# Kernel tuning notes

Measured on AMD Instinct MI355X. Metric: run time of the kernel, lower is better.

## Reference

```python
import jax, jax.numpy as jnp
import numpy as np

HIDDEN = 1024
NUM_HEADS = 4
HEAD_DIM = HIDDEN // NUM_HEADS
SCALE = HEAD_DIM ** -0.5
EPS = 1e-5


def setup_inputs() -> dict:
    key = jax.random.key(0)
    ks = jax.random.split(key, 8)
    B, S, D = 4, 2048, HIDDEN
    x = jax.random.normal(ks[0], (B, S, D), dtype=jnp.float32)
    attention_mask = jnp.ones((B, S), dtype=jnp.int32)
    init = 1.0 / np.sqrt(D)
    Wq = jax.random.uniform(ks[1], (D, D), jnp.float32, -init, init)
    Wk = jax.random.uniform(ks[2], (D, D), jnp.float32, -init, init)
    Wv = jax.random.uniform(ks[3], (D, D), jnp.float32, -init, init)
    Wo = jax.random.uniform(ks[4], (D, D), jnp.float32, -init, init)
    bo = jax.random.uniform(ks[5], (D,), jnp.float32, -init, init)
    gamma = jnp.ones((D,), dtype=jnp.float32)
    beta = jnp.zeros((D,), dtype=jnp.float32)
    return {"x": x, "attention_mask": attention_mask, "Wq": Wq, "Wk": Wk,
            "Wv": Wv, "Wo": Wo, "bo": bo, "gamma": gamma, "beta": beta}


def reference(x, attention_mask, Wq, Wk, Wv, Wo, bo, gamma, beta):
    # Linear layers: y = x @ W^T (torch nn.Linear convention), no bias for q/k/v
    q = jnp.einsum('bsd,ed->bse', x, Wq)
    k = jnp.einsum('bsd,ed->bse', x, Wk)
    v = jnp.einsum('bsd,ed->bse', x, Wv)
    # Full-width attention (module never splits heads), scale = head_dim^-0.5
    scores = jnp.einsum('bqd,bkd->bqk', q, k) * SCALE  # [B,S,S]
    mask = attention_mask[:, None, :]  # [B,1,S]
    scores = jnp.where(mask == 0, jnp.float32(-1e9), scores)
    attn = jax.nn.softmax(scores, axis=-1)
    ctx = jnp.einsum('bqk,bkd->bqd', attn, v)
    out = jnp.einsum('bsd,ed->bse', ctx, Wo) + bo
    # residual + LayerNorm
    h = out + x
    mu = jnp.mean(h, axis=-1, keepdims=True)
    var = jnp.mean(jnp.square(h - mu), axis=-1, keepdims=True)
    return (h - mu) * jax.lax.rsqrt(var + EPS) * gamma + beta
```

## Files before the change

### kernel.cpp

```cpp
#include <hip/hip_runtime.h>

typedef __bf16 bf16;
typedef __bf16 bf16x8 __attribute__((ext_vector_type(8)));
typedef __bf16 bf16x4 __attribute__((ext_vector_type(4)));
typedef float floatx4 __attribute__((ext_vector_type(4)));

#define HIDDEN 1024
#define SEQ 2048
#define BATCH 4
#define ATT_SCALE 0.0625f
#define LN_EPS 1e-5f

__device__ __forceinline__ void gload_lds16(const void* g, void* l) {
    __builtin_amdgcn_global_load_lds(
        (const __attribute__((address_space(1))) unsigned int*)g,
        (__attribute__((address_space(3))) unsigned int*)l, 16, 0, 0);
}

#define GBAR() asm volatile("s_barrier" ::: "memory")
#define MFMA(a, b, c) __builtin_amdgcn_mfma_f32_16x16x32_bf16(a, b, c, 0, 0, 0)

__global__ void cvt_f32_bf16(const float* __restrict__ in, bf16* __restrict__ out, int n4) {
    int i = blockIdx.x * blockDim.x + threadIdx.x;
    if (i >= n4) return;
    float4 v = ((const float4*)in)[i];
    bf16x4 o;
    o[0] = (bf16)v.x; o[1] = (bf16)v.y; o[2] = (bf16)v.z; o[3] = (bf16)v.w;
    ((bf16x4*)out)[i] = o;
}

__global__ void transpose_w3(const float* __restrict__ s0, const float* __restrict__ s1,
                             const float* __restrict__ s2,
                             bf16* __restrict__ d0p, bf16* __restrict__ d1p, bf16* __restrict__ d2p) {
    const float* in = (blockIdx.z == 0) ? s0 : (blockIdx.z == 1) ? s1 : s2;
    bf16* out = (blockIdx.z == 0) ? d0p : (blockIdx.z == 1) ? d1p : d2p;
    __shared__ __attribute__((aligned(16))) bf16 tile[64][72];
    const int d0 = blockIdx.x * 64;
    const int f0 = blockIdx.y * 64;
    const int t = threadIdx.x;
    const int r = t >> 4;
    const int c = (t & 15) * 4;
#pragma unroll
    for (int i = 0; i < 4; ++i) {
        float4 v = *(const float4*)&in[(long)(f0 + r + i * 16) * HIDDEN + d0 + c];
        bf16x4 b;
        b[0] = (bf16)v.x; b[1] = (bf16)v.y; b[2] = (bf16)v.z; b[3] = (bf16)v.w;
        *(bf16x4*)&tile[r + i * 16][c] = b;
    }
    __syncthreads();
#pragma unroll
    for (int i = 0; i < 4; ++i) {
        const int dr = r + i * 16;
        bf16x4 o;
#pragma unroll
        for (int j = 0; j < 4; ++j) o[j] = tile[c + j][dr];
        *(bf16x4*)&out[(long)(d0 + dr) * HIDDEN + f0 + c] = o;
    }
}

template <int BNv, int MODE>
__global__ __launch_bounds__(512, 2)
void gemm256(const bf16* A, const bf16* Bw, void* __restrict__ Cout,
             const float* __restrict__ bias, const float* __restrict__ resid,
             int lda, int ldb, int ldc, int K, float scale,
             long sA, long sB, long sC) {
    constexpr int ABY = 256 * 128;
    constexpr int BBY = BNv * 128;
    constexpr int SLOT = ABY + BBY;
    constexpr int AU = ABY / 8192;
    constexpr int BU = BBY / 8192;
    constexpr int WNc = (BNv == 256) ? 4 : 2;
    constexpr int MR = (BNv == 256) ? 8 : 4;
    constexpr int MH = MR / 2;

    __shared__ __attribute__((aligned(16))) char lds[2 * SLOT];

    const int gx = gridDim.x;
    const int nblk = gx * gridDim.y;
    const int bid = blockIdx.y * gx + blockIdx.x;
    const int cpx = nblk >> 3;
    const int sbid = (nblk & 7) ? bid : (bid & 7) * cpx + (bid >> 3);
    const int bx = sbid % gx, by = sbid / gx;

    const int z = blockIdx.z;
    const char* Ab = (const char*)(A + (long)z * sA);
    const char* Bb = (const char*)(Bw + (long)z * sB);
    const long lda2 = lda * 2L, ldb2 = ldb * 2L;

    const int t = threadIdx.x;
    const int lane = t & 63;
    const int w = t >> 6;
    const int wm = w / WNc, wn = w % WNc;
    const int l15 = lane & 15;
    const int l4 = lane >> 4;

    const int row0 = by * 256;
    const int col0 = bx * BNv;

    const int srow = t >> 3;
    const int soff = (((t & 7) - (srow & 7)) & 7) * 16;
    const char* aP = Ab + (long)(row0 + srow) * lda2 + soff;
    const char* bP = Bb + (long)(col0 + srow) * ldb2 + soff;
    const int ld16 = t * 16;

    auto STAGE = [&](int slot, long koff) {
        char* base = &lds[slot * SLOT];
#pragma unroll
        for (int u = 0; u < AU; ++u)
            gload_lds16(aP + u * 64 * lda2 + koff, base + u * 8192 + ld16);
#pragma unroll
        for (int u = 0; u < BU; ++u)
            gload_lds16(bP + u * 64 * ldb2 + koff, base + ABY + u * 8192 + ld16);
    };

    floatx4 acc[MR][4] = {};
    const int nk = K / 64;

    STAGE(0, 0);
    asm volatile("s_waitcnt vmcnt(0)" ::: "memory");
    GBAR();

    for (int tt = 0; tt < nk; ++tt) {
        const char* sb = &lds[(tt & 1) * SLOT];

        auto RDA = [&](int m, int kkh) {
            int lr = wm * (MR * 16) + m * 16 + l15;
            return *(const bf16x8*)(sb + lr * 128 + (((kkh * 4 + l4 + lr) & 7) << 4));
        };
        auto RDB = [&](int n, int kkh) {
            int lr = wn * 64 + n * 16 + l15;
            return *(const bf16x8*)(sb + ABY + lr * 128 + (((kkh * 4 + l4 + lr) & 7) << 4));
        };

        bf16x8 alo[MH][2], ahi[MH][2], b0[2][2], b1[2][2];
#pragma unroll
        for (int m = 0; m < MH; ++m) { alo[m][0] = RDA(m, 0); alo[m][1] = RDA(m, 1); }
#pragma unroll
        for (int n = 0; n < 2; ++n) {
            b0[n][0] = RDB(n, 0); b0[n][1] = RDB(n, 1);
            b1[n][0] = RDB(2 + n, 0); b1[n][1] = RDB(2 + n, 1);
        }

        if (tt + 1 < nk) STAGE((tt + 1) & 1, (long)(tt + 1) * 128);

        __builtin_amdgcn_s_setprio(1);
#pragma unroll
        for (int m = 0; m < MH; ++m)
#pragma unroll
            for (int n = 0; n < 2; ++n) {
                acc[m][n] = MFMA(alo[m][0], b0[n][0], acc[m][n]);
                acc[m][n] = MFMA(alo[m][1], b0[n][1], acc[m][n]);
            }
        __builtin_amdgcn_s_setprio(0);

#pragma unroll
        for (int m = 0; m < MH; ++m) { ahi[m][0] = RDA(MH + m, 0); ahi[m][1] = RDA(MH + m, 1); }

        __builtin_amdgcn_s_setprio(1);
#pragma unroll
        for (int m = 0; m < MH; ++m)
#pragma unroll
            for (int n = 0; n < 2; ++n) {
                acc[m][2 + n] = MFMA(alo[m][0], b1[n][0], acc[m][2 + n]);
                acc[m][2 + n] = MFMA(alo[m][1], b1[n][1], acc[m][2 + n]);
            }
#pragma unroll
        for (int m = 0; m < MH; ++m)
#pragma unroll
            for (int n = 0; n < 2; ++n) {
                acc[MH + m][n] = MFMA(ahi[m][0], b0[n][0], acc[MH + m][n]);
                acc[MH + m][n] = MFMA(ahi[m][1], b0[n][1], acc[MH + m][n]);
            }
#pragma unroll
        for (int m = 0; m < MH; ++m)
#pragma unroll
            for (int n = 0; n < 2; ++n) {
                acc[MH + m][2 + n] = MFMA(ahi[m][0], b1[n][0], acc[MH + m][2 + n]);
                acc[MH + m][2 + n] = MFMA(ahi[m][1], b1[n][1], acc[MH + m][2 + n]);
            }
        __builtin_amdgcn_s_setprio(0);

        asm volatile("s_waitcnt vmcnt(0)" ::: "memory");
        GBAR();
    }

    const int rq = l4 * 4;
    if constexpr (MODE == 0) {
        bf16* C = ((bf16*)Cout) + (long)z * sC;
#pragma unroll
        for (int m = 0; m < MR; ++m)
#pragma unroll
            for (int i = 0; i < 4; ++i) {
                long gr = row0 + wm * (MR * 16) + m * 16 + rq + i;
#pragma unroll
                for (int n = 0; n < 4; ++n) {
                    int gc = col0 + wn * 64 + n * 16 + l15;
                    C[gr * ldc + gc] = (bf16)(acc[m][n][i] * scale);
                }
            }
    } else {
        float* C = (float*)Cout + (long)z * sC;
        const float* R = resid + (long)z * sC;
#pragma unroll
        for (int m = 0; m < MR; ++m)
#pragma unroll
            for (int i = 0; i < 4; ++i) {
                long gr = row0 + wm * (MR * 16) + m * 16 + rq + i;
#pragma unroll
                for (int n = 0; n < 4; ++n) {
                    int gc = col0 + wn * 64 + n * 16 + l15;
                    C[gr * ldc + gc] = acc[m][n][i] + bias[gc] + R[gr * ldc + gc];
                }
            }
    }
}

__global__ void transpose_v(const bf16* __restrict__ yv, bf16* __restrict__ out) {
    __shared__ __attribute__((aligned(16))) bf16 tile[64][72];
    const int z = blockIdx.z;
    const bf16* ib = yv + (long)z * SEQ * 2048 + 1024;
    bf16* ob = out + (long)z * SEQ * HIDDEN;
    const int d0 = blockIdx.x * 64;
    const int s0 = blockIdx.y * 64;
    const int t = threadIdx.x;
    const int r = t >> 4;
    const int c = (t & 15) * 4;
#pragma unroll
    for (int i = 0; i < 4; ++i) {
        bf16x4 v = *(const bf16x4*)&ib[(long)(s0 + r + i * 16) * 2048 + d0 + c];
        *(bf16x4*)&tile[r + i * 16][c] = v;
    }
    __syncthreads();
#pragma unroll
    for (int i = 0; i < 4; ++i) {
        const int dr = r + i * 16;
        bf16x4 o;
#pragma unroll
        for (int j = 0; j < 4; ++j) o[j] = tile[c + j][dr];
        *(bf16x4*)&ob[(long)(d0 + dr) * SEQ + s0 + c] = o;
    }
}

__global__ void softmax_rows(bf16* __restrict__ S, const int* __restrict__ mask) {
    const int b = blockIdx.y;
    const int row = blockIdx.x;
    bf16* srow = S + ((long)b * SEQ + row) * SEQ;
    const int* mrow = mask + b * SEQ;
    const int t = threadIdx.x;

    bf16x8 sv = *(const bf16x8*)&srow[t * 8];
    int4 m0 = ((const int4*)mrow)[t * 2];
    int4 m1 = ((const int4*)mrow)[t * 2 + 1];
    int mk[8] = {m0.x, m0.y, m0.z, m0.w, m1.x, m1.y, m1.z, m1.w};

    float v[8];
    float mx = -1e30f;
#pragma unroll
    for (int j = 0; j < 8; ++j) {
        float s = (float)sv[j];
        if (mk[j] == 0) s = -1e9f;
        v[j] = s;
        mx = fmaxf(mx, s);
    }
    __shared__ float redm[4], reds[4];
#pragma unroll
    for (int off = 32; off > 0; off >>= 1) mx = fmaxf(mx, __shfl_down(mx, off));
    if ((t & 63) == 0) redm[t >> 6] = mx;
    __syncthreads();
    mx = fmaxf(fmaxf(redm[0], redm[1]), fmaxf(redm[2], redm[3]));

    float sum = 0.f;
#pragma unroll
    for (int j = 0; j < 8; ++j) {
        v[j] = __expf(v[j] - mx);
        sum += v[j];
    }
#pragma unroll
    for (int off = 32; off > 0; off >>= 1) sum += __shfl_down(sum, off);
    if ((t & 63) == 0) reds[t >> 6] = sum;
    __syncthreads();
    sum = reds[0] + reds[1] + reds[2] + reds[3];
    float inv = 1.0f / sum;

    bf16x8 o;
#pragma unroll
    for (int j = 0; j < 8; ++j) o[j] = (bf16)(v[j] * inv);
    *(bf16x8*)&srow[t * 8] = o;
}

__global__ void layernorm_out(const float* __restrict__ h, const float* __restrict__ gamma,
                              const float* __restrict__ beta, float* __restrict__ out) {
    const long row = blockIdx.x;
    const float* hr = h + row * HIDDEN;
    const int t = threadIdx.x;
    float4 v = ((const float4*)hr)[t];
    float s = v.x + v.y + v.z + v.w;
    float sq = v.x * v.x + v.y * v.y + v.z * v.z + v.w * v.w;
    __shared__ float rs[4], rq[4];
#pragma unroll
    for (int off = 32; off > 0; off >>= 1) {
        s += __shfl_down(s, off);
        sq += __shfl_down(sq, off);
    }
    if ((t & 63) == 0) { rs[t >> 6] = s; rq[t >> 6] = sq; }
    __syncthreads();
    s = rs[0] + rs[1] + rs[2] + rs[3];
    sq = rq[0] + rq[1] + rq[2] + rq[3];
    float mu = s * (1.0f / HIDDEN);
    float var = sq * (1.0f / HIDDEN) - mu * mu;
    float rinv = rsqrtf(var + LN_EPS);
    float4 g = ((const float4*)gamma)[t];
    float4 bt = ((const float4*)beta)[t];
    float4 o;
    o.x = (v.x - mu) * rinv * g.x + bt.x;
    o.y = (v.y - mu) * rinv * g.y + bt.y;
    o.z = (v.z - mu) * rinv * g.z + bt.z;
    o.w = (v.w - mu) * rinv * g.w + bt.w;
    ((float4*)(out + row * HIDDEN))[t] = o;
}

extern "C" void kernel_launch(void* const* d_in, const int* in_sizes, int n_in,
                              void* d_out, int out_size, void* d_ws, size_t ws_size,
                              hipStream_t stream) {
    const float* x     = (const float*)d_in[0];
    const int*   mask  = (const int*)d_in[1];
    const float* Wq    = (const float*)d_in[2];
    const float* Wk    = (const float*)d_in[3];
    const float* Wv    = (const float*)d_in[4];
    const float* Wo    = (const float*)d_in[5];
    const float* bo    = (const float*)d_in[6];
    const float* gamma = (const float*)d_in[7];
    const float* beta  = (const float*)d_in[8];
    float* out = (float*)d_out;

    char* ws = (char*)d_ws;
    const long MB = 1024L * 1024L;
    bf16* yv   = (bf16*)(ws + 0 * MB);
    float* h   = (float*)(ws + 0 * MB);
    bf16* xb   = (bf16*)(ws + 32 * MB);
    bf16* vt   = (bf16*)(ws + 48 * MB);
    bf16* wgc  = (bf16*)(ws + 64 * MB);
    bf16* wkT  = (bf16*)(ws + 68 * MB);
    bf16* wo   = (bf16*)(ws + 70 * MB);
    bf16* wqT  = (bf16*)(ws + 72 * MB);
    bf16* wvT  = (bf16*)(ws + 74 * MB);
    bf16* S    = (bf16*)(ws + 76 * MB);

    const int BS = BATCH * SEQ;
    const int WW = HIDDEN * HIDDEN;
    dim3 blk256(256), blk512(512);

    cvt_f32_bf16<<<dim3(BS * HIDDEN / 4 / 256), blk256, 0, stream>>>(x, xb, BS * HIDDEN / 4);
    cvt_f32_bf16<<<dim3(WW / 4 / 256), blk256, 0, stream>>>(Wo, wo, WW / 4);
    transpose_w3<<<dim3(16, 16, 3), blk256, 0, stream>>>(Wq, Wk, Wv, wqT, wkT, wvT);

    gemm256<128, 0><<<dim3(HIDDEN / 128, HIDDEN / 256, 2), blk512, 0, stream>>>(
        wkT, wqT, wgc, nullptr, nullptr, HIDDEN, HIDDEN, HIDDEN, HIDDEN, 1.0f,
        (long)WW, (long)WW, (long)WW);

    gemm256<256, 0><<<dim3(2048 / 256, BS / 256, 1), blk512, 0, stream>>>(
        xb, wgc, yv, nullptr, nullptr, HIDDEN, HIDDEN, 2048, HIDDEN, 1.0f, 0, 0, 0);

    transpose_v<<<dim3(HIDDEN / 64, SEQ / 64, BATCH), blk256, 0, stream>>>(yv, vt);

    gemm256<256, 0><<<dim3(SEQ / 256, SEQ / 256, BATCH), blk512, 0, stream>>>(
        yv, xb, S, nullptr, nullptr, 2048, HIDDEN, SEQ, HIDDEN, ATT_SCALE,
        (long)SEQ * 2048, (long)SEQ * HIDDEN, (long)SEQ * SEQ);

    softmax_rows<<<dim3(SEQ, BATCH), blk256, 0, stream>>>(S, mask);

    gemm256<128, 2><<<dim3(HIDDEN / 128, SEQ / 256, BATCH), blk512, 0, stream>>>(
        S, vt, h, bo, x, SEQ, SEQ, HIDDEN, SEQ, 1.0f,
        (long)SEQ * SEQ, (long)HIDDEN * SEQ, (long)SEQ * HIDDEN);

    layernorm_out<<<dim3(BS), blk256, 0, stream>>>(h, gamma, beta, out);
}
```

Before: 181.3 us.

## Split-K the weight-product and PV GEMMs, move bias and residual into LayerNorm

The Wk^T·Wq product GEMM is split four ways along K into fp32 partials, which a new reduce kernel sums into bf16. The attention-times-V GEMM is split in two along K, writing bf16 partials. The bias, residual add and partial summation move into the LayerNorm kernel. The goal is more blocks for under-filled grids on many CUs, at the cost of extra partial-buffer traffic, an extra launch, and bf16 rounding of the partials.

```diff
diff --git a/kernel.cpp b/kernel.cpp
--- a/kernel.cpp
+++ b/kernel.cpp
@@ -10,6 +10,7 @@
 #define BATCH 4
 #define ATT_SCALE 0.0625f
 #define LN_EPS 1e-5f
+#define WW (HIDDEN * HIDDEN)
 
 __device__ __forceinline__ void gload_lds16(const void* g, void* l) {
     __builtin_amdgcn_global_load_lds(
@@ -61,9 +62,8 @@
 template <int BNv, int MODE>
 __global__ __launch_bounds__(512, 2)
 void gemm256(const bf16* A, const bf16* Bw, void* __restrict__ Cout,
-             const float* __restrict__ bias, const float* __restrict__ resid,
              int lda, int ldb, int ldc, int K, float scale,
-             long sA, long sB, long sC) {
+             long sA, long sB, long sC, int zmod) {
     constexpr int ABY = 256 * 128;
     constexpr int BBY = BNv * 128;
     constexpr int SLOT = ABY + BBY;
@@ -83,8 +83,9 @@
     const int bx = sbid % gx, by = sbid / gx;
 
     const int z = blockIdx.z;
-    const char* Ab = (const char*)(A + (long)z * sA);
-    const char* Bb = (const char*)(Bw + (long)z * sB);
+    const int mat = z % zmod, ks = z / zmod;
+    const char* Ab = (const char*)(A + (long)mat * sA + (long)ks * K);
+    const char* Bb = (const char*)(Bw + (long)mat * sB + (long)ks * K);
     const long lda2 = lda * 2L, ldb2 = ldb * 2L;
 
     const int t = threadIdx.x;
@@ -200,7 +201,6 @@
             }
     } else {
         float* C = (float*)Cout + (long)z * sC;
-        const float* R = resid + (long)z * sC;
 #pragma unroll
         for (int m = 0; m < MR; ++m)
 #pragma unroll
@@ -209,10 +209,73 @@
 #pragma unroll
                 for (int n = 0; n < 4; ++n) {
                     int gc = col0 + wn * 64 + n * 16 + l15;
-                    C[gr * ldc + gc] = acc[m][n][i] + bias[gc] + R[gr * ldc + gc];
+                    C[gr * ldc + gc] = acc[m][n][i];
                 }
             }
     }
+}
+
+__global__ void reduce_wgc(const float* __restrict__ p, bf16* __restrict__ out) {
+    int i = blockIdx.x * blockDim.x + threadIdx.x;
+    int e = i * 4;
+    int mat = e >> 20;
+    int local = e & (WW - 1);
+    float4 s = *(const float4*)(p + (long)mat * WW + local);
+#pragma unroll
+    for (int ksp = 1; ksp < 4; ++ksp) {
+        float4 a = *(const float4*)(p + (long)(ksp * 2 + mat) * WW + local);
+        s.x += a.x; s.y += a.y; s.z += a.z; s.w += a.w;
+    }
+    bf16x4 o;
+    o[0] = (bf16)s.x; o[1] = (bf16)s.y; o[2] = (bf16)s.z; o[3] = (bf16)s.w;
+    *(bf16x4*)&out[e] = o;
+}
+
+__global__ void softmax_rows(bf16* __restrict__ S, const int* __restrict__ mask) {
+    const int b = blockIdx.y;
+    const int row = blockIdx.x;
+    bf16* srow = S + ((long)b * SEQ + row) * SEQ;
+    const int* mrow = mask + b * SEQ;
+    const int t = threadIdx.x;
+
+    bf16x8 sv = *(const bf16x8*)&srow[t * 8];
+    int4 m0 = ((const int4*)mrow)[t * 2];
+    int4 m1 = ((const int4*)mrow)[t * 2 + 1];
+    int mk[8] = {m0.x, m0.y, m0.z, m0.w, m1.x, m1.y, m1.z, m1.w};
+
+    float v[8];
+    float mx = -1e30f;
+#pragma unroll
+    for (int j = 0; j < 8; ++j) {
+        float s = (float)sv[j];
+        if (mk[j] == 0) s = -1e9f;
+        v[j] = s;
+        mx = fmaxf(mx, s);
+    }
+    __shared__ float redm[4], reds[4];
+#pragma unroll
+    for (int off = 32; off > 0; off >>= 1) mx = fmaxf(mx, __shfl_down(mx, off));
+    if ((t & 63) == 0) redm[t >> 6] = mx;
+    __syncthreads();
+    mx = fmaxf(fmaxf(redm[0], redm[1]), fmaxf(redm[2], redm[3]));
+
+    float sum = 0.f;
+#pragma unroll
+    for (int j = 0; j < 8; ++j) {
+        v[j] = __expf(v[j] - mx);
+        sum += v[j];
+    }
+#pragma unroll
+    for (int off = 32; off > 0; off >>= 1) sum += __shfl_down(sum, off);
+    if ((t & 63) == 0) reds[t >> 6] = sum;
+    __syncthreads();
+    sum = reds[0] + reds[1] + reds[2] + reds[3];
+    float inv = 1.0f / sum;
+
+    bf16x8 o;
+#pragma unroll
+    for (int j = 0; j < 8; ++j) o[j] = (bf16)(v[j] * inv);
+    *(bf16x8*)&srow[t * 8] = o;
 }
 
 __global__ void transpose_v(const bf16* __restrict__ yv, bf16* __restrict__ out) {
@@ -241,72 +304,39 @@
     }
 }
 
-__global__ void softmax_rows(bf16* __restrict__ S, const int* __restrict__ mask) {
-    const int b = blockIdx.y;
-    const int row = blockIdx.x;
-    bf16* srow = S + ((long)b * SEQ + row) * SEQ;
-    const int* mrow = mask + b * SEQ;
-    const int t = threadIdx.x;
-
-    bf16x8 sv = *(const bf16x8*)&srow[t * 8];
-    int4 m0 = ((const int4*)mrow)[t * 2];
-    int4 m1 = ((const int4*)mrow)[t * 2 + 1];
-    int mk[8] = {m0.x, m0.y, m0.z, m0.w, m1.x, m1.y, m1.z, m1.w};
-
-    float v[8];
-    float mx = -1e30f;
-#pragma unroll
-    for (int j = 0; j < 8; ++j) {
-        float s = (float)sv[j];
-        if (mk[j] == 0) s = -1e9f;
-        v[j] = s;
-        mx = fmaxf(mx, s);
-    }
-    __shared__ float redm[4], reds[4];
-#pragma unroll
-    for (int off = 32; off > 0; off >>= 1) mx = fmaxf(mx, __shfl_down(mx, off));
-    if ((t & 63) == 0) redm[t >> 6] = mx;
-    __syncthreads();
-    mx = fmaxf(fmaxf(redm[0], redm[1]), fmaxf(redm[2], redm[3]));
-
-    float sum = 0.f;
-#pragma unroll
-    for (int j = 0; j < 8; ++j) {
-        v[j] = __expf(v[j] - mx);
-        sum += v[j];
-    }
-#pragma unroll
-    for (int off = 32; off > 0; off >>= 1) sum += __shfl_down(sum, off);
-    if ((t & 63) == 0) reds[t >> 6] = sum;
-    __syncthreads();
-    sum = reds[0] + reds[1] + reds[2] + reds[3];
-    float inv = 1.0f / sum;
-
-    bf16x8 o;
-#pragma unroll
-    for (int j = 0; j < 8; ++j) o[j] = (bf16)(v[j] * inv);
-    *(bf16x8*)&srow[t * 8] = o;
-}
-
-__global__ void layernorm_out(const float* __restrict__ h, const float* __restrict__ gamma,
+__global__ void layernorm_out(const bf16* __restrict__ pp, const float* __restrict__ x,
+                              const float* __restrict__ bo, const float* __restrict__ gamma,
                               const float* __restrict__ beta, float* __restrict__ out) {
     const long row = blockIdx.x;
-    const float* hr = h + row * HIDDEN;
+    const int b = (int)(row >> 11);
+    const int s = (int)(row & 2047);
+    const bf16* r0 = pp + ((long)b * SEQ + s) * HIDDEN;
+    const bf16* r1 = r0 + 4L * SEQ * HIDDEN;
     const int t = threadIdx.x;
-    float4 v = ((const float4*)hr)[t];
-    float s = v.x + v.y + v.z + v.w;
+
+    bf16x4 a0 = ((const bf16x4*)r0)[t];
+    bf16x4 a1 = ((const bf16x4*)r1)[t];
+    float4 xv = ((const float4*)(x + row * HIDDEN))[t];
+    float4 bv = ((const float4*)bo)[t];
+    float4 v;
+    v.x = (float)a0[0] + (float)a1[0] + bv.x + xv.x;
+    v.y = (float)a0[1] + (float)a1[1] + bv.y + xv.y;
+    v.z = (float)a0[2] + (float)a1[2] + bv.z + xv.z;
+    v.w = (float)a0[3] + (float)a1[3] + bv.w + xv.w;
+
+    float ssum = v.x + v.y + v.z + v.w;
     float sq = v.x * v.x + v.y * v.y + v.z * v.z + v.w * v.w;
     __shared__ float rs[4], rq[4];
 #pragma unroll
     for (int off = 32; off > 0; off >>= 1) {
-        s += __shfl_down(s, off);
+        ssum += __shfl_down(ssum, off);
         sq += __shfl_down(sq, off);
     }
-    if ((t & 63) == 0) { rs[t >> 6] = s; rq[t >> 6] = sq; }
+    if ((t & 63) == 0) { rs[t >> 6] = ssum; rq[t >> 6] = sq; }
     __syncthreads();
-    s = rs[0] + rs[1] + rs[2] + rs[3];
+    ssum = rs[0] + rs[1] + rs[2] + rs[3];
     sq = rq[0] + rq[1] + rq[2] + rq[3];
-    float mu = s * (1.0f / HIDDEN);
+    float mu = ssum * (1.0f / HIDDEN);
     float var = sq * (1.0f / HIDDEN) - mu * mu;
     float rinv = rsqrtf(var + LN_EPS);
     float4 g = ((const float4*)gamma)[t];
@@ -336,7 +366,7 @@
     char* ws = (char*)d_ws;
     const long MB = 1024L * 1024L;
     bf16* yv   = (bf16*)(ws + 0 * MB);
-    float* h   = (float*)(ws + 0 * MB);
+    bf16* pp   = (bf16*)(ws + 0 * MB);
     bf16* xb   = (bf16*)(ws + 32 * MB);
     bf16* vt   = (bf16*)(ws + 48 * MB);
     bf16* wgc  = (bf16*)(ws + 64 * MB);
@@ -345,33 +375,34 @@
     bf16* wqT  = (bf16*)(ws + 72 * MB);
     bf16* wvT  = (bf16*)(ws + 74 * MB);
     bf16* S    = (bf16*)(ws + 76 * MB);
+    float* wgcp = (float*)(ws + 76 * MB);
 
     const int BS = BATCH * SEQ;
-    const int WW = HIDDEN * HIDDEN;
     dim3 blk256(256), blk512(512);
 
     cvt_f32_bf16<<<dim3(BS * HIDDEN / 4 / 256), blk256, 0, stream>>>(x, xb, BS * HIDDEN / 4);
     cvt_f32_bf16<<<dim3(WW / 4 / 256), blk256, 0, stream>>>(Wo, wo, WW / 4);
     transpose_w3<<<dim3(16, 16, 3), blk256, 0, stream>>>(Wq, Wk, Wv, wqT, wkT, wvT);
 
-    gemm256<128, 0><<<dim3(HIDDEN / 128, HIDDEN / 256, 2), blk512, 0, stream>>>(
-        wkT, wqT, wgc, nullptr, nullptr, HIDDEN, HIDDEN, HIDDEN, HIDDEN, 1.0f,
-        (long)WW, (long)WW, (long)WW);
+    gemm256<128, 4><<<dim3(HIDDEN / 128, HIDDEN / 256, 8), blk512, 0, stream>>>(
+        wkT, wqT, wgcp, HIDDEN, HIDDEN, HIDDEN, 256, 1.0f,
+        (long)WW, (long)WW, (long)WW, 2);
+    reduce_wgc<<<dim3(2 * WW / 4 / 256), blk256, 0, stream>>>(wgcp, wgc);
 
     gemm256<256, 0><<<dim3(2048 / 256, BS / 256, 1), blk512, 0, stream>>>(
-        xb, wgc, yv, nullptr, nullptr, HIDDEN, HIDDEN, 2048, HIDDEN, 1.0f, 0, 0, 0);
+        xb, wgc, yv, HIDDEN, HIDDEN, 2048, HIDDEN, 1.0f, 0, 0, 0, 1);
 
     transpose_v<<<dim3(HIDDEN / 64, SEQ / 64, BATCH), blk256, 0, stream>>>(yv, vt);
 
     gemm256<256, 0><<<dim3(SEQ / 256, SEQ / 256, BATCH), blk512, 0, stream>>>(
-        yv, xb, S, nullptr, nullptr, 2048, HIDDEN, SEQ, HIDDEN, ATT_SCALE,
-        (long)SEQ * 2048, (long)SEQ * HIDDEN, (long)SEQ * SEQ);
+        yv, xb, S, 2048, HIDDEN, SEQ, HIDDEN, ATT_SCALE,
+        (long)SEQ * 2048, (long)SEQ * HIDDEN, (long)SEQ * SEQ, 4);
 
     softmax_rows<<<dim3(SEQ, BATCH), blk256, 0, stream>>>(S, mask);
 
-    gemm256<128, 2><<<dim3(HIDDEN / 128, SEQ / 256, BATCH), blk512, 0, stream>>>(
-        S, vt, h, bo, x, SEQ, SEQ, HIDDEN, SEQ, 1.0f,
-        (long)SEQ * SEQ, (long)HIDDEN * SEQ, (long)SEQ * HIDDEN);
-
-    layernorm_out<<<dim3(BS), blk256, 0, stream>>>(h, gamma, beta, out);
-}
+    gemm256<128, 0><<<dim3(HIDDEN / 128, SEQ / 256, 8), blk512, 0, stream>>>(
+        S, vt, pp, SEQ, SEQ, HIDDEN, 1024, 1.0f,
+        (long)SEQ * SEQ, (long)HIDDEN * SEQ, (long)SEQ * HIDDEN, 4);
+
+    layernorm_out<<<dim3(BS), blk256, 0, stream>>>(pp, x, bo, gamma, beta, out);
+}
```

New measurement: 187.9 us. 3.6% more time.
